# Performance work log

Measured on AMD Instinct MI355X. Metric: run time of the kernel, lower is better.

The kernel has to match this reference:

```python
import jax, jax.numpy as jnp
import numpy as np

N, D, K = 131072, 64, 4096


def setup_inputs() -> dict:
    key = jax.random.key(0)
    k1, k2 = jax.random.split(key)
    x = jax.random.normal(k1, (N, D), dtype=jnp.float32)
    embed = jax.random.normal(k2, (K, D), dtype=jnp.float32)
    return {"x": x, "embed": embed}


def reference(x, embed):
    """EuclideanCodebook forward.

    x:     [N, D] flat input vectors
    embed: [K, D] codebook
    Returns (quantize [N,D], embed_ind [N], cluster_size [K], embed_sum [K,D]).
    cluster_size / embed_sum are the one-hot scatter statistics fed to the
    EMA codebook update (embed_onehot.sum(0) and flatten^T @ embed_onehot).
    """
    num_codes = embed.shape[0]
    x2 = jnp.sum(x * x, axis=-1, keepdims=True)               # [N, 1]
    e2 = jnp.sum(embed * embed, axis=-1)                      # [K]
    dist = x2 - 2.0 * (x @ embed.T) + e2[None, :]             # [N, K]
    embed_ind = jnp.argmin(dist, axis=-1)                     # [N]
    quantize = embed[embed_ind]                               # gather [N, D]
    # scatter statistics for EMA update
    cluster_size = jnp.zeros((num_codes,), x.dtype).at[embed_ind].add(1.0)  # [K]
    embed_sum = jax.ops.segment_sum(x, embed_ind, num_segments=num_codes)   # [K, D]
    return quantize, embed_ind, cluster_size, embed_sum
```

## Files before the change

kernel.cpp:

```cpp
#include <hip/hip_runtime.h>

#define N_ROWS 131072
#define DIM 64
#define K_CODES 4096
#define BROWS 256
#define CK 64
#define NCH (K_CODES / CK)
#define EST 72
#define EPS 0.015625f
#define HEPS 0.0078125f

typedef __attribute__((ext_vector_type(8))) short short8;
typedef __attribute__((ext_vector_type(4))) float f32x4;

__device__ inline unsigned short bf16rn(float f) {
    unsigned int u = __float_as_uint(f);
    u += 0x7FFFu + ((u >> 16) & 1u);
    return (unsigned short)(u >> 16);
}
__device__ inline unsigned int fkey(float f) {
    unsigned int u = __float_as_uint(f);
    return (u & 0x80000000u) ? ~u : (u | 0x80000000u);
}

__global__ void pack_kernel(const float* __restrict__ embed,
                            unsigned short* __restrict__ ebf,
                            float* __restrict__ e2,
                            float* __restrict__ e2h,
                            int* __restrict__ cnt,
                            float* __restrict__ cs) {
    const int g = blockIdx.x * blockDim.x + threadIdx.x;
    for (int i = g; i < K_CODES + K_CODES * DIM; i += K_CODES * 16)
        cs[i] = 0.f;
    if (g == 0) *cnt = 0;

    const int code = g >> 4;
    const int w    = g & 15;
    const int half = w >> 3;
    const int d0   = (w & 7) << 3;
    const float* ep = embed + (size_t)code * DIM + d0;
    float4 f0 = *(const float4*)ep;
    float4 f1 = *(const float4*)(ep + 4);
    float wv[8] = {f0.x, f0.y, f0.z, f0.w, f1.x, f1.y, f1.z, f1.w};
    unsigned short o[8];
    float ssq = 0.f;
#pragma unroll
    for (int j = 0; j < 8; ++j) {
        unsigned short hb = bf16rn(wv[j]);
        if (half == 0) {
            o[j] = hb;
            ssq = fmaf(wv[j], wv[j], ssq);
        } else {
            float hf = __uint_as_float(((unsigned int)hb) << 16);
            o[j] = bf16rn(wv[j] - hf);
        }
    }
    *(uint4*)(ebf + (size_t)code * 128 + half * 64 + d0) = *(uint4*)o;
    ssq += __shfl_xor(ssq, 1, 64);
    ssq += __shfl_xor(ssq, 2, 64);
    ssq += __shfl_xor(ssq, 4, 64);
    if (w == 0) {
        e2[code]  = ssq;
        e2h[code] = -0.5f * ssq;
    }
}

__global__ __launch_bounds__(512, 4) void dist_argmin_kernel(
        const float* __restrict__ x, const unsigned short* __restrict__ ebf,
        const float* __restrict__ e2h, const float* __restrict__ embed,
        int* __restrict__ ind_ws, float* __restrict__ ind_out,
        int* __restrict__ cnt, int* __restrict__ list,
        float* __restrict__ quant, float* __restrict__ cs,
        float* __restrict__ esum, int fused) {
    __shared__ unsigned short esh[2][CK * EST];
    __shared__ unsigned short esl[2][CK * EST];
    __shared__ float e2s[2][CK];

    const int tid  = threadIdx.x;
    const int l15  = tid & 15;
    const int quad = (tid >> 4) & 3;
    const int wave = tid >> 6;
    const int r0w  = blockIdx.x * BROWS + wave * 32;

    const int col = tid >> 3;
    const int dq  = (tid & 7) * 8;

    uint4 sh0, sl0;
    float se2 = 0.f;
    {
        const unsigned short* pp = ebf + (size_t)col * 128 + dq;
        sh0 = *(const uint4*)pp;
        sl0 = *(const uint4*)(pp + 64);
        if (tid < CK) se2 = e2h[tid];
    }

    short8 ah[2][2], al[2][2];
#pragma unroll
    for (int i = 0; i < 2; ++i)
#pragma unroll
        for (int s = 0; s < 2; ++s) {
            const float* xp = x + (size_t)(r0w + 16 * i + l15) * DIM + 32 * s + 8 * quad;
            float4 f0 = *(const float4*)xp;
            float4 f1 = *(const float4*)(xp + 4);
            float w[8] = {f0.x, f0.y, f0.z, f0.w, f1.x, f1.y, f1.z, f1.w};
            short8 h, l;
#pragma unroll
            for (int j = 0; j < 8; ++j) {
                unsigned short hb = bf16rn(w[j]);
                float hf = __uint_as_float(((unsigned int)hb) << 16);
                h[j] = (short)hb;
                l[j] = (short)bf16rn(w[j] - hf);
            }
            ah[i][s] = h;
            al[i][s] = l;
        }

    *(uint4*)(&esh[0][col * EST + dq]) = sh0;
    *(uint4*)(&esl[0][col * EST + dq]) = sl0;
    if (tid < CK) e2s[0][tid] = se2;

    float s1[8], s2[8];
    int c1[8];
#pragma unroll
    for (int t = 0; t < 8; ++t) { s1[t] = -3.4e38f; s2[t] = -3.4e38f; c1[t] = 0; }

    __syncthreads();

    int cur = 0;
    for (int ch = 0; ch < NCH; ++ch) {
        {
            const int c0n = ((ch + 1) & (NCH - 1)) * CK;
            const unsigned short* pp = ebf + (size_t)(c0n + col) * 128 + dq;
            sh0 = *(const uint4*)pp;
            sl0 = *(const uint4*)(pp + 64);
            if (tid < CK) se2 = e2h[c0n + tid];
        }

        const int c0 = ch * CK;

        f32x4 acc[2][4];
#pragma unroll
        for (int j = 0; j < 4; ++j) {
            const float ev = e2s[cur][16 * j + l15];
            const f32x4 iv = {ev, ev, ev, ev};
#pragma unroll
            for (int i = 0; i < 2; ++i) acc[i][j] = iv;
        }

#pragma unroll
        for (int j = 0; j < 4; ++j) {
            const int cb = (16 * j + l15) * EST + 8 * quad;
            short8 bh0 = *(const short8*)(&esh[cur][cb]);
            short8 bh1 = *(const short8*)(&esh[cur][cb + 32]);
            short8 bl0 = *(const short8*)(&esl[cur][cb]);
            short8 bl1 = *(const short8*)(&esl[cur][cb + 32]);
#pragma unroll
            for (int i = 0; i < 2; ++i) {
                f32x4 a = acc[i][j];
                a = __builtin_amdgcn_mfma_f32_16x16x32_bf16(ah[i][0], bh0, a, 0, 0, 0);
                a = __builtin_amdgcn_mfma_f32_16x16x32_bf16(ah[i][1], bh1, a, 0, 0, 0);
                a = __builtin_amdgcn_mfma_f32_16x16x32_bf16(ah[i][0], bl0, a, 0, 0, 0);
                a = __builtin_amdgcn_mfma_f32_16x16x32_bf16(ah[i][1], bl1, a, 0, 0, 0);
                a = __builtin_amdgcn_mfma_f32_16x16x32_bf16(al[i][0], bh0, a, 0, 0, 0);
                a = __builtin_amdgcn_mfma_f32_16x16x32_bf16(al[i][1], bh1, a, 0, 0, 0);
                acc[i][j] = a;
            }
        }

#pragma unroll
        for (int j = 0; j < 4; ++j) {
            const int c = c0 + 16 * j + l15;
#pragma unroll
            for (int i = 0; i < 2; ++i)
#pragma unroll
                for (int r = 0; r < 4; ++r) {
                    float d = acc[i][j][r];
                    const int st = i * 4 + r;
                    bool gt = d > s1[st];
                    s2[st] = fmaxf(fminf(d, s1[st]), s2[st]);
                    c1[st] = gt ? c : c1[st];
                    s1[st] = fmaxf(s1[st], d);
                }
        }

        const int nxt = cur ^ 1;
        *(uint4*)(&esh[nxt][col * EST + dq]) = sh0;
        *(uint4*)(&esl[nxt][col * EST + dq]) = sl0;
        if (tid < CK) e2s[nxt][tid] = se2;

        __syncthreads();
        cur = nxt;
    }

#pragma unroll
    for (int st = 0; st < 8; ++st) {
#pragma unroll
        for (int m = 1; m < 16; m <<= 1) {
            float os1 = __shfl_xor(s1[st], m, 64);
            float os2 = __shfl_xor(s2[st], m, 64);
            int   oc1 = __shfl_xor(c1[st], m, 64);
            bool take = (os1 > s1[st]) || (os1 == s1[st] && oc1 < c1[st]);
            float loser = take ? s1[st] : os1;
            s2[st] = fmaxf(fmaxf(s2[st], os2), loser);
            if (take) { s1[st] = os1; c1[st] = oc1; }
        }
    }
    if (l15 == 0) {
#pragma unroll
        for (int st = 0; st < 8; ++st) {
            const int i = st >> 2, r = st & 3;
            const int row = r0w + 16 * i + 4 * quad + r;
            ind_ws[row] = c1[st];
            ind_out[row] = (float)c1[st];
            if (s1[st] - s2[st] < HEPS) {
                int p = atomicAdd(cnt, 1);
                list[p] = row;
            }
        }
    }

    if (fused) {
        int* li = (int*)&esh[0][0];
        if (l15 == 0) {
#pragma unroll
            for (int st = 0; st < 8; ++st) {
                const int i = st >> 2, r = st & 3;
                li[(wave << 5) + 16 * i + 4 * quad + r] = c1[st];
            }
        }
        const int lane = tid & 63;
        for (int t = 0; t < 32; ++t) {
            const int k = li[(wave << 5) + t];
            const size_t row = (size_t)(r0w + t);
            quant[row * DIM + lane] = embed[(size_t)k * DIM + lane];
            float xv = x[row * DIM + lane];
            atomicAdd(&esum[(size_t)k * DIM + lane], xv);
            if (lane == 0) atomicAdd(&cs[k], 1.0f);
        }
    }
}

__global__ void refine_kernel(const float* __restrict__ x,
                              const float* __restrict__ embed,
                              const float* __restrict__ e2g,
                              const int* __restrict__ cnt,
                              const int* __restrict__ list,
                              int* __restrict__ ind_ws,
                              float* __restrict__ ind_out,
                              float* __restrict__ quant,
                              float* __restrict__ cs,
                              float* __restrict__ esum, int fused) {
    __shared__ float xr[DIM];
    __shared__ unsigned long long red[256];
    const int tid = threadIdx.x;
    const int n = *cnt;
    for (int f = blockIdx.x; f < n; f += gridDim.x) {
        const int row = list[f];
        __syncthreads();
        if (tid < 16)
            ((float4*)xr)[tid] = ((const float4*)(x + (size_t)row * DIM))[tid];
        __syncthreads();
        unsigned long long best = ~0ull;
        for (int c = tid; c < K_CODES; c += 256) {
            const float4* ep = (const float4*)(embed + (size_t)c * DIM);
            float d0 = 0.f, d1 = 0.f, d2 = 0.f, d3 = 0.f;
#pragma unroll
            for (int q = 0; q < 16; ++q) {
                float4 ev = ep[q];
                d0 = fmaf(xr[4 * q + 0], ev.x, d0);
                d1 = fmaf(xr[4 * q + 1], ev.y, d1);
                d2 = fmaf(xr[4 * q + 2], ev.z, d2);
                d3 = fmaf(xr[4 * q + 3], ev.w, d3);
            }
            float sc = fmaf(-2.f, (d0 + d1) + (d2 + d3), e2g[c]);
            unsigned long long key =
                ((unsigned long long)fkey(sc) << 32) | (unsigned int)c;
            if (key < best) best = key;
        }
        red[tid] = best;
        __syncthreads();
        for (int w = 128; w > 0; w >>= 1) {
            if (tid < w && red[tid + w] < red[tid]) red[tid] = red[tid + w];
            __syncthreads();
        }
        const int k_new = (int)(red[0] & 0xFFFFFFFFull);
        if (fused) {
            const int k_old = ind_ws[row];
            if (k_new != k_old) {
                if (tid < DIM) {
                    float xv = xr[tid];
                    atomicAdd(&esum[(size_t)k_old * DIM + tid], -xv);
                    atomicAdd(&esum[(size_t)k_new * DIM + tid],  xv);
                    quant[(size_t)row * DIM + tid] =
                        embed[(size_t)k_new * DIM + tid];
                }
                if (tid == 0) {
                    atomicAdd(&cs[k_old], -1.f);
                    atomicAdd(&cs[k_new],  1.f);
                    ind_ws[row] = k_new;
                    ind_out[row] = (float)k_new;
                }
            }
        } else if (tid == 0) {
            ind_ws[row] = k_new;
            ind_out[row] = (float)k_new;
        }
    }
}

__global__ void scatter_kernel(const float* __restrict__ x,
                               const float* __restrict__ embed,
                               const int* __restrict__ ind,
                               float* __restrict__ quant,
                               float* __restrict__ cs,
                               float* __restrict__ esum) {
    const int t = blockIdx.x * blockDim.x + threadIdx.x;
    const int row = t >> 6;
    const int d = t & 63;
    const int k = ind[row];
    quant[t] = embed[(size_t)k * DIM + d];
    atomicAdd(&esum[(size_t)k * DIM + d], x[t]);
    if (d == 0) atomicAdd(&cs[k], 1.0f);
}

extern "C" void kernel_launch(void* const* d_in, const int* in_sizes, int n_in,
                              void* d_out, int out_size, void* d_ws, size_t ws_size,
                              hipStream_t stream) {
    const float* x     = (const float*)d_in[0];
    const float* embed = (const float*)d_in[1];

    float* out     = (float*)d_out;
    float* quant   = out;
    float* ind_out = out + (size_t)N_ROWS * DIM;
    float* cs      = ind_out + N_ROWS;
    float* esum    = cs + K_CODES;

    float* e2   = (float*)d_ws;
    int* cnt    = (int*)(e2 + K_CODES);
    int* list   = cnt + 4;
    int* ind_ws = list + N_ROWS;
    float* e2h  = (float*)(ind_ws + N_ROWS);
    unsigned short* ebf_ws = (unsigned short*)(e2h + K_CODES);
    const size_t ws_need =
        (size_t)((char*)(ebf_ws + (size_t)K_CODES * 128) - (char*)d_ws);

    const int fused = (ws_size >= ws_need) ? 1 : 0;
    unsigned short* ebf = fused ? ebf_ws : (unsigned short*)quant;

    pack_kernel<<<(K_CODES * 16) / 256, 256, 0, stream>>>(
        embed, ebf, e2, e2h, cnt, cs);
    dist_argmin_kernel<<<N_ROWS / BROWS, 512, 0, stream>>>(
        x, ebf, e2h, embed, ind_ws, ind_out, cnt, list, quant, cs, esum, fused);
    refine_kernel<<<512, 256, 0, stream>>>(
        x, embed, e2, cnt, list, ind_ws, ind_out, quant, cs, esum, fused);
    if (!fused)
        scatter_kernel<<<(size_t)N_ROWS * DIM / 256, 256, 0, stream>>>(
            x, embed, ind_ws, quant, cs, esum);
}
```

Baseline: 412.8 us.

## Load codebook B-fragments directly from global into registers, drop LDS staging

The distance kernel no longer stages codebook chunks in double-buffered shared memory with a block-wide barrier per chunk. Each wave now loads its bf16 hi/lo MFMA B-operands and e2 terms straight from global memory (L2-resident) into registers, prefetching the next chunk after the MFMAs. Block size drops to 256 threads with 128 rows per block. This removes LDS traffic and syncs, but raises register pressure and means every wave re-fetches the whole codebook from cache, which puts more load on L2/L1 bandwidth.

```diff
diff --git a/kernel.cpp b/kernel.cpp
--- a/kernel.cpp
+++ b/kernel.cpp
@@ -3,10 +3,9 @@
 #define N_ROWS 131072
 #define DIM 64
 #define K_CODES 4096
-#define BROWS 256
+#define BROWS 128
 #define CK 64
 #define NCH (K_CODES / CK)
-#define EST 72
 #define EPS 0.015625f
 #define HEPS 0.0078125f
 
@@ -65,16 +64,14 @@
     }
 }
 
-__global__ __launch_bounds__(512, 4) void dist_argmin_kernel(
+__global__ __launch_bounds__(256, 2) void dist_argmin_kernel(
         const float* __restrict__ x, const unsigned short* __restrict__ ebf,
         const float* __restrict__ e2h, const float* __restrict__ embed,
         int* __restrict__ ind_ws, float* __restrict__ ind_out,
         int* __restrict__ cnt, int* __restrict__ list,
         float* __restrict__ quant, float* __restrict__ cs,
         float* __restrict__ esum, int fused) {
-    __shared__ unsigned short esh[2][CK * EST];
-    __shared__ unsigned short esl[2][CK * EST];
-    __shared__ float e2s[2][CK];
+    __shared__ int li[4][32];
 
     const int tid  = threadIdx.x;
     const int l15  = tid & 15;
@@ -82,17 +79,27 @@
     const int wave = tid >> 6;
     const int r0w  = blockIdx.x * BROWS + wave * 32;
 
-    const int col = tid >> 3;
-    const int dq  = (tid & 7) * 8;
-
-    uint4 sh0, sl0;
-    float se2 = 0.f;
-    {
-        const unsigned short* pp = ebf + (size_t)col * 128 + dq;
-        sh0 = *(const uint4*)pp;
-        sl0 = *(const uint4*)(pp + 64);
-        if (tid < CK) se2 = e2h[tid];
-    }
+    const int voff = l15 * 128 + quad * 8;
+
+    short8 bh0[4], bh1[4], bl0[4], bl1[4];
+    float e2v[4];
+
+#define LOADB(CH) do {                                                       \
+        const unsigned short* _b = ebf + (size_t)(CH) * 8192 + voff;         \
+        _Pragma("unroll")                                                    \
+        for (int _j = 0; _j < 4; ++_j) {                                     \
+            const short8* _p = (const short8*)(_b + _j * 2048);              \
+            bh0[_j] = _p[0];                \
+            bh1[_j] = _p[4];                \
+            bl0[_j] = _p[8];                \
+            bl1[_j] = _p[12];               \
+        }                                                                    \
+        const float* _e = e2h + (size_t)(CH) * CK + l15;                     \
+        _Pragma("unroll")                                                    \
+        for (int _j = 0; _j < 4; ++_j) e2v[_j] = _e[16 * _j];                \
+    } while (0)
+
+    LOADB(0);
 
     short8 ah[2][2], al[2][2];
 #pragma unroll
@@ -115,57 +122,38 @@
             al[i][s] = l;
         }
 
-    *(uint4*)(&esh[0][col * EST + dq]) = sh0;
-    *(uint4*)(&esl[0][col * EST + dq]) = sl0;
-    if (tid < CK) e2s[0][tid] = se2;
-
     float s1[8], s2[8];
     int c1[8];
 #pragma unroll
     for (int t = 0; t < 8; ++t) { s1[t] = -3.4e38f; s2[t] = -3.4e38f; c1[t] = 0; }
 
-    __syncthreads();
-
-    int cur = 0;
     for (int ch = 0; ch < NCH; ++ch) {
-        {
-            const int c0n = ((ch + 1) & (NCH - 1)) * CK;
-            const unsigned short* pp = ebf + (size_t)(c0n + col) * 128 + dq;
-            sh0 = *(const uint4*)pp;
-            sl0 = *(const uint4*)(pp + 64);
-            if (tid < CK) se2 = e2h[c0n + tid];
-        }
-
         const int c0 = ch * CK;
 
         f32x4 acc[2][4];
 #pragma unroll
         for (int j = 0; j < 4; ++j) {
-            const float ev = e2s[cur][16 * j + l15];
+            const float ev = e2v[j];
             const f32x4 iv = {ev, ev, ev, ev};
-#pragma unroll
-            for (int i = 0; i < 2; ++i) acc[i][j] = iv;
-        }
-
-#pragma unroll
-        for (int j = 0; j < 4; ++j) {
-            const int cb = (16 * j + l15) * EST + 8 * quad;
-            short8 bh0 = *(const short8*)(&esh[cur][cb]);
-            short8 bh1 = *(const short8*)(&esh[cur][cb + 32]);
-            short8 bl0 = *(const short8*)(&esl[cur][cb]);
-            short8 bl1 = *(const short8*)(&esl[cur][cb + 32]);
+            acc[0][j] = iv;
+            acc[1][j] = iv;
+        }
+
+#pragma unroll
+        for (int j = 0; j < 4; ++j)
 #pragma unroll
             for (int i = 0; i < 2; ++i) {
                 f32x4 a = acc[i][j];
-                a = __builtin_amdgcn_mfma_f32_16x16x32_bf16(ah[i][0], bh0, a, 0, 0, 0);
-                a = __builtin_amdgcn_mfma_f32_16x16x32_bf16(ah[i][1], bh1, a, 0, 0, 0);
-                a = __builtin_amdgcn_mfma_f32_16x16x32_bf16(ah[i][0], bl0, a, 0, 0, 0);
-                a = __builtin_amdgcn_mfma_f32_16x16x32_bf16(ah[i][1], bl1, a, 0, 0, 0);
-                a = __builtin_amdgcn_mfma_f32_16x16x32_bf16(al[i][0], bh0, a, 0, 0, 0);
-                a = __builtin_amdgcn_mfma_f32_16x16x32_bf16(al[i][1], bh1, a, 0, 0, 0);
+                a = __builtin_amdgcn_mfma_f32_16x16x32_bf16(ah[i][0], bh0[j], a, 0, 0, 0);
+                a = __builtin_amdgcn_mfma_f32_16x16x32_bf16(ah[i][1], bh1[j], a, 0, 0, 0);
+                a = __builtin_amdgcn_mfma_f32_16x16x32_bf16(ah[i][0], bl0[j], a, 0, 0, 0);
+                a = __builtin_amdgcn_mfma_f32_16x16x32_bf16(ah[i][1], bl1[j], a, 0, 0, 0);
+                a = __builtin_amdgcn_mfma_f32_16x16x32_bf16(al[i][0], bh0[j], a, 0, 0, 0);
+                a = __builtin_amdgcn_mfma_f32_16x16x32_bf16(al[i][1], bh1[j], a, 0, 0, 0);
                 acc[i][j] = a;
             }
-        }
+
+        LOADB((ch + 1) & (NCH - 1));
 
 #pragma unroll
         for (int j = 0; j < 4; ++j) {
@@ -182,15 +170,8 @@
                     s1[st] = fmaxf(s1[st], d);
                 }
         }
-
-        const int nxt = cur ^ 1;
-        *(uint4*)(&esh[nxt][col * EST + dq]) = sh0;
-        *(uint4*)(&esl[nxt][col * EST + dq]) = sl0;
-        if (tid < CK) e2s[nxt][tid] = se2;
-
-        __syncthreads();
-        cur = nxt;
-    }
+    }
+#undef LOADB
 
 #pragma unroll
     for (int st = 0; st < 8; ++st) {
@@ -220,17 +201,16 @@
     }
 
     if (fused) {
-        int* li = (int*)&esh[0][0];
         if (l15 == 0) {
 #pragma unroll
             for (int st = 0; st < 8; ++st) {
                 const int i = st >> 2, r = st & 3;
-                li[(wave << 5) + 16 * i + 4 * quad + r] = c1[st];
+                li[wave][16 * i + 4 * quad + r] = c1[st];
             }
         }
         const int lane = tid & 63;
         for (int t = 0; t < 32; ++t) {
-            const int k = li[(wave << 5) + t];
+            const int k = li[wave][t];
             const size_t row = (size_t)(r0w + t);
             quant[row * DIM + lane] = embed[(size_t)k * DIM + lane];
             float xv = x[row * DIM + lane];
@@ -349,7 +329,7 @@
 
     pack_kernel<<<(K_CODES * 16) / 256, 256, 0, stream>>>(
         embed, ebf, e2, e2h, cnt, cs);
-    dist_argmin_kernel<<<N_ROWS / BROWS, 512, 0, stream>>>(
+    dist_argmin_kernel<<<N_ROWS / BROWS, 256, 0, stream>>>(
         x, ebf, e2h, embed, ind_ws, ind_out, cnt, list, quant, cs, esum, fused);
     refine_kernel<<<512, 256, 0, stream>>>(
         x, embed, e2, cnt, list, ind_ws, ind_out, quant, cs, esum, fused);
```

Result: slower. 655.5 us (+58.8%).
